# Optimization experiments

Hardware: AMD Instinct MI355X
Metric: run time of the kernel (lower is better)

The kernel has to match this reference:

```python
import jax, jax.numpy as jnp
import numpy as np

I, H = 1, 16  # input_size, hidden_size


def setup_inputs() -> dict:
    key = jax.random.key(0)
    ks = jax.random.split(key, 7)
    B, T = 8192, 512
    s_ih = 1.0 / np.sqrt(H)
    return {
        "x": jax.random.normal(ks[0], (B, T, I), dtype=jnp.float32),
        "W_ih": jax.random.uniform(ks[1], (3 * H, I), minval=-s_ih, maxval=s_ih, dtype=jnp.float32),
        "W_hh": jax.random.uniform(ks[2], (3 * H, H), minval=-s_ih, maxval=s_ih, dtype=jnp.float32),
        "b_ih": jax.random.uniform(ks[3], (3 * H,), minval=-s_ih, maxval=s_ih, dtype=jnp.float32),
        "b_hh": jax.random.uniform(ks[4], (3 * H,), minval=-s_ih, maxval=s_ih, dtype=jnp.float32),
        "fc_w": jax.random.uniform(ks[5], (1, H), minval=-s_ih, maxval=s_ih, dtype=jnp.float32),
        "fc_b": jax.random.uniform(ks[6], (1,), minval=-s_ih, maxval=s_ih, dtype=jnp.float32),
    }


def _gru_last_hidden(x, W_ih, W_hh, b_ih, b_hh):
    # Precompute input projections for all timesteps: [B, T, 3H]
    xp = jnp.einsum("bti,gi->btg", x, W_ih) + b_ih
    xp = jnp.transpose(xp, (1, 0, 2))  # [T, B, 3H] for scan over time
    B = x.shape[0]
    h0 = jnp.zeros((B, H), dtype=x.dtype)

    def step(h, xt):
        # PyTorch GRU gate equations (gate order: r, z, n)
        gh = h @ W_hh.T + b_hh  # [B, 3H]
        xr, xz, xn = xt[:, :H], xt[:, H:2 * H], xt[:, 2 * H:]
        hr, hz, hn = gh[:, :H], gh[:, H:2 * H], gh[:, 2 * H:]
        r = jax.nn.sigmoid(xr + hr)
        z = jax.nn.sigmoid(xz + hz)
        n = jnp.tanh(xn + r * hn)
        h_new = (1.0 - z) * n + z * h
        return h_new, None

    h_last, _ = jax.lax.scan(step, h0, xp)
    return h_last  # [B, H]


def reference(x, W_ih, W_hh, b_ih, b_hh, fc_w, fc_b):
    # Dropout is identity in eval mode
    h_last = _gru_last_hidden(x, W_ih, W_hh, b_ih, b_hh)
    return h_last @ fc_w.T + fc_b  # [B, 1]
```

## Files before the change

kernel.cpp:

```cpp
#include <hip/hip_runtime.h>

namespace {

constexpr int T_LEN = 512;
constexpr float LOG2E = 1.4426950408889634f;

typedef _Float16 half4 __attribute__((ext_vector_type(4)));
typedef _Float16 half2v __attribute__((ext_vector_type(2)));
typedef float v4f __attribute__((ext_vector_type(4)));

__device__ __forceinline__ float fexp2(float a) {
#if __has_builtin(__builtin_amdgcn_exp2f)
    return __builtin_amdgcn_exp2f(a);
#else
    return exp2f(a);
#endif
}

__device__ __forceinline__ v4f mfma16h(half4 a, half4 b, v4f c) {
#if __has_builtin(__builtin_amdgcn_mfma_f32_16x16x16f16)
    return __builtin_amdgcn_mfma_f32_16x16x16f16(a, b, c, 0, 0, 0);
#else
    v4f d;
    asm volatile("v_mfma_f32_16x16x16_f16 %0, %1, %2, %3\n\ts_nop 7\n\ts_nop 7"
                 : "=v"(d) : "v"(a), "v"(b), "v"(c));
    return d;
#endif
}

__device__ __forceinline__ unsigned pk_f16(float a, float b) {
#if __has_builtin(__builtin_amdgcn_cvt_pkrtz)
    return __builtin_bit_cast(unsigned, __builtin_amdgcn_cvt_pkrtz(a, b));
#else
    half2v r; r[0] = (_Float16)a; r[1] = (_Float16)b;
    return __builtin_bit_cast(unsigned, r);
#endif
}

template<int CTRL>
__device__ __forceinline__ unsigned dpp_mov_u(unsigned v) {
    return (unsigned)__builtin_amdgcn_mov_dpp((int)v, CTRL, 0xF, 0xF, false);
}

__device__ __forceinline__ float gru_pair(float drp, float dzp, float dnp,
                                          float xt, float wihn, float bihn,
                                          float hp) {
    float Er = fexp2(drp);
    float Ez = fexp2(dzp);
    float pr = 1.0f + Er;
    float pz = 1.0f + Ez;
    float ip = __builtin_amdgcn_rcpf(pr * pz);
    float r  = ip * pz;
    float z  = ip * pr;
    float xn = __builtin_fmaf(xt, wihn, bihn);
    float v  = __builtin_fmaf(r, dnp, xn);
    float n  = __builtin_fmaf(-2.0f, __builtin_amdgcn_rcpf(1.0f + fexp2(v)), 1.0f);
    return __builtin_fmaf(z, hp - n, n);
}

__global__ __launch_bounds__(64) void gru_mfma8d(
        const float* __restrict__ x,
        const float* __restrict__ W_ih,
        const float* __restrict__ W_hh,
        const float* __restrict__ b_ih,
        const float* __restrict__ b_hh,
        const float* __restrict__ fc_w,
        const float* __restrict__ fc_b,
        float* __restrict__ out) {
    const int L  = threadIdx.x;
    const int e  = L & 15;
    const int g  = L >> 4;
    const int jD = g * 4;
    const int ehi  = (e >> 3) & 1;
    const int ecol = e & 7;
    const int be   = blockIdx.x * 8 + ecol;
    const int r0   = jD + 2 * ehi;

    const float sR = -LOG2E;
    const float sN = 2.0f * LOG2E;

    half4 ar_h, az_h, an_h;
#pragma unroll
    for (int i = 0; i < 4; ++i) {
        ar_h[i] = (_Float16)(W_hh[(0  + e) * 16 + jD + i] * sR);
        az_h[i] = (_Float16)(W_hh[(16 + e) * 16 + jD + i] * sR);
        an_h[i] = (_Float16)(W_hh[(32 + e) * 16 + jD + i] * sN);
    }

    v4f c_r, c_z, c_n;
#pragma unroll
    for (int i = 0; i < 4; ++i) {
        int rj = jD + i;
        c_r[i] = (b_ih[rj]      + b_hh[rj])      * sR;
        c_z[i] = (b_ih[16 + rj] + b_hh[16 + rj]) * sR;
        c_n[i] = b_hh[32 + rj] * sN;
    }
    const float wihr0 = W_ih[r0]          * sR, wihr1 = W_ih[r0 + 1]      * sR;
    const float wihz0 = W_ih[16 + r0]     * sR, wihz1 = W_ih[16 + r0 + 1] * sR;
    const float wihn0 = W_ih[32 + r0]     * sN, wihn1 = W_ih[32 + r0 + 1] * sN;
    const float bihn0 = b_ih[32 + r0]     * sN, bihn1 = b_ih[32 + r0 + 1] * sN;

    const float4* xb = (const float4*)(x + (size_t)be * T_LEN);
    float4 xc0 = xb[0], xc1 = xb[1], xc2 = xb[2], xc3 = xb[3];

    float hp0 = 0.f, hp1 = 0.f;
    uint2 hz; hz.x = 0u; hz.y = 0u;
    half4 hf = __builtin_bit_cast(half4, hz);

#pragma unroll 1
    for (int c = 0; c < T_LEN / 16; ++c) {
        float4 xn0, xn1, xn2, xn3;
        if (c + 1 < T_LEN / 16) {
            xn0 = xb[(c + 1) * 4 + 0];
            xn1 = xb[(c + 1) * 4 + 1];
            xn2 = xb[(c + 1) * 4 + 2];
            xn3 = xb[(c + 1) * 4 + 3];
        }
#pragma unroll
        for (int s = 0; s < 16; ++s) {
            float4 q4 = (s < 4) ? xc0 : (s < 8) ? xc1 : (s < 12) ? xc2 : xc3;
            float xt  = ((s & 3) == 0) ? q4.x : ((s & 3) == 1) ? q4.y
                      : ((s & 3) == 2) ? q4.z : q4.w;

            v4f dr = mfma16h(ar_h, hf, c_r);
            v4f dz = mfma16h(az_h, hf, c_z);
            v4f dn = mfma16h(an_h, hf, c_n);

            float d_r0 = __builtin_fmaf(xt, wihr0, ehi ? dr[2] : dr[0]);
            float d_r1 = __builtin_fmaf(xt, wihr1, ehi ? dr[3] : dr[1]);
            float d_z0 = __builtin_fmaf(xt, wihz0, ehi ? dz[2] : dz[0]);
            float d_z1 = __builtin_fmaf(xt, wihz1, ehi ? dz[3] : dz[1]);
            float d_n0 = ehi ? dn[2] : dn[0];
            float d_n1 = ehi ? dn[3] : dn[1];

            float h0n = gru_pair(d_r0, d_z0, d_n0, xt, wihn0, bihn0, hp0);
            float h1n = gru_pair(d_r1, d_z1, d_n1, xt, wihn1, bihn1, hp1);
            hp0 = h0n; hp1 = h1n;

            unsigned mine = pk_f16(h0n, h1n);
            unsigned oth  = dpp_mov_u<0x128>(mine);
            uint2 hv;
            hv.x = ehi ? oth  : mine;
            hv.y = ehi ? mine : oth;
            hf = __builtin_bit_cast(half4, hv);
        }
        if (c + 1 < T_LEN / 16) { xc0 = xn0; xc1 = xn1; xc2 = xn2; xc3 = xn3; }
    }

    float p = hp0 * fc_w[r0] + hp1 * fc_w[r0 + 1];
    p += __shfl_xor(p, 8, 64);
    p += __shfl_xor(p, 16, 64);
    p += __shfl_xor(p, 32, 64);
    if (L < 8) out[blockIdx.x * 8 + L] = p + fc_b[0];
}

}

extern "C" void kernel_launch(void* const* d_in, const int* in_sizes, int n_in,
                              void* d_out, int out_size, void* d_ws, size_t ws_size,
                              hipStream_t stream) {
    const float* x    = (const float*)d_in[0];
    const float* W_ih = (const float*)d_in[1];
    const float* W_hh = (const float*)d_in[2];
    const float* b_ih = (const float*)d_in[3];
    const float* b_hh = (const float*)d_in[4];
    const float* fc_w = (const float*)d_in[5];
    const float* fc_b = (const float*)d_in[6];
    float* out = (float*)d_out;

    const int B = out_size;
    const int blocks = B / 8;
    gru_mfma8d<<<blocks, 64, 0, stream>>>(x, W_ih, W_hh, b_ih, b_hh,
                                          fc_w, fc_b, out);
}
```

Baseline: 87.68 us.

## Map one hidden unit per lane with 4 batch columns per wave

Each wave now processes 4 batch sequences instead of 8, so each lane computes a single hidden unit per step rather than two, and the grid doubles. The hidden-state transpose back into MFMA B-operand layout uses three DPP row shifts plus selects, with a runtime probe that detects the shift direction. This shortens the per-step serial gate chain and adds more waves to hide latency, at the cost of doubling total MFMA issue per batch element and adding more cross-lane moves.

```diff
diff --git a/kernel.cpp b/kernel.cpp
--- a/kernel.cpp
+++ b/kernel.cpp
@@ -38,8 +38,15 @@
 }
 
 template<int CTRL>
-__device__ __forceinline__ unsigned dpp_mov_u(unsigned v) {
-    return (unsigned)__builtin_amdgcn_mov_dpp((int)v, CTRL, 0xF, 0xF, false);
+__device__ __forceinline__ float dpp_mov_f(float v) {
+    return __builtin_bit_cast(float,
+        __builtin_amdgcn_mov_dpp(__builtin_bit_cast(int, v), CTRL, 0xF, 0xF, false));
+}
+
+__device__ __forceinline__ float sel4(v4f d, bool qb0, bool qb1) {
+    float a = qb0 ? d[1] : d[0];
+    float b = qb0 ? d[3] : d[2];
+    return qb1 ? b : a;
 }
 
 __device__ __forceinline__ float gru_pair(float drp, float dzp, float dnp,
@@ -58,7 +65,7 @@
     return __builtin_fmaf(z, hp - n, n);
 }
 
-__global__ __launch_bounds__(64) void gru_mfma8d(
+__global__ __launch_bounds__(64) void gru_mfma4d(
         const float* __restrict__ x,
         const float* __restrict__ W_ih,
         const float* __restrict__ W_hh,
@@ -71,10 +78,15 @@
     const int e  = L & 15;
     const int g  = L >> 4;
     const int jD = g * 4;
-    const int ehi  = (e >> 3) & 1;
-    const int ecol = e & 7;
-    const int be   = blockIdx.x * 8 + ecol;
-    const int r0   = jD + 2 * ehi;
+    const int q    = (e >> 2) & 3;
+    const bool qb0 = (q & 1) != 0;
+    const bool qb1 = (q & 2) != 0;
+    const int ecol = e & 3;
+    const int be   = blockIdx.x * 4 + ecol;
+    const int rme  = jD + q;
+
+    const int tprobe = __builtin_amdgcn_mov_dpp(e, 0x124, 0xF, 0xF, false);
+    const bool flip = (((tprobe - e) & 15) != 4);
 
     const float sR = -LOG2E;
     const float sN = 2.0f * LOG2E;
@@ -95,15 +107,15 @@
         c_z[i] = (b_ih[16 + rj] + b_hh[16 + rj]) * sR;
         c_n[i] = b_hh[32 + rj] * sN;
     }
-    const float wihr0 = W_ih[r0]          * sR, wihr1 = W_ih[r0 + 1]      * sR;
-    const float wihz0 = W_ih[16 + r0]     * sR, wihz1 = W_ih[16 + r0 + 1] * sR;
-    const float wihn0 = W_ih[32 + r0]     * sN, wihn1 = W_ih[32 + r0 + 1] * sN;
-    const float bihn0 = b_ih[32 + r0]     * sN, bihn1 = b_ih[32 + r0 + 1] * sN;
+    const float wihr_s = W_ih[rme]      * sR;
+    const float wihz_s = W_ih[16 + rme] * sR;
+    const float wihn_s = W_ih[32 + rme] * sN;
+    const float bihn_s = b_ih[32 + rme] * sN;
 
     const float4* xb = (const float4*)(x + (size_t)be * T_LEN);
     float4 xc0 = xb[0], xc1 = xb[1], xc2 = xb[2], xc3 = xb[3];
 
-    float hp0 = 0.f, hp1 = 0.f;
+    float hp = 0.f;
     uint2 hz; hz.x = 0u; hz.y = 0u;
     half4 hf = __builtin_bit_cast(half4, hz);
 
@@ -126,32 +138,40 @@
             v4f dz = mfma16h(az_h, hf, c_z);
             v4f dn = mfma16h(an_h, hf, c_n);
 
-            float d_r0 = __builtin_fmaf(xt, wihr0, ehi ? dr[2] : dr[0]);
-            float d_r1 = __builtin_fmaf(xt, wihr1, ehi ? dr[3] : dr[1]);
-            float d_z0 = __builtin_fmaf(xt, wihz0, ehi ? dz[2] : dz[0]);
-            float d_z1 = __builtin_fmaf(xt, wihz1, ehi ? dz[3] : dz[1]);
-            float d_n0 = ehi ? dn[2] : dn[0];
-            float d_n1 = ehi ? dn[3] : dn[1];
+            float d_r = __builtin_fmaf(xt, wihr_s, sel4(dr, qb0, qb1));
+            float d_z = __builtin_fmaf(xt, wihz_s, sel4(dz, qb0, qb1));
+            float d_n = sel4(dn, qb0, qb1);
+            float hn = gru_pair(d_r, d_z, d_n, xt, wihn_s, bihn_s, hp);
+            hp = hn;
 
-            float h0n = gru_pair(d_r0, d_z0, d_n0, xt, wihn0, bihn0, hp0);
-            float h1n = gru_pair(d_r1, d_z1, d_n1, xt, wihn1, bihn1, hp1);
-            hp0 = h0n; hp1 = h1n;
-
-            unsigned mine = pk_f16(h0n, h1n);
-            unsigned oth  = dpp_mov_u<0x128>(mine);
+            float v0 = hn;
+            float v1 = dpp_mov_f<0x124>(hn);
+            float v2 = dpp_mov_f<0x128>(hn);
+            float v3 = dpp_mov_f<0x12C>(hn);
+            float t1 = flip ? v3 : v1;
+            float t3 = flip ? v1 : v3;
+            float a0 = qb0 ? t3 : v0, b0 = qb0 ? t1 : v2;
+            float row0 = qb1 ? b0 : a0;
+            float a1 = qb0 ? v0 : t1, b1 = qb0 ? v2 : t3;
+            float row1 = qb1 ? b1 : a1;
+            float a2 = qb0 ? t1 : v2, b2 = qb0 ? t3 : v0;
+            float row2 = qb1 ? b2 : a2;
+            float a3 = qb0 ? v2 : t3, b3 = qb0 ? v0 : t1;
+            float row3 = qb1 ? b3 : a3;
             uint2 hv;
-            hv.x = ehi ? oth  : mine;
-            hv.y = ehi ? mine : oth;
+            hv.x = pk_f16(row0, row1);
+            hv.y = pk_f16(row2, row3);
             hf = __builtin_bit_cast(half4, hv);
         }
         if (c + 1 < T_LEN / 16) { xc0 = xn0; xc1 = xn1; xc2 = xn2; xc3 = xn3; }
     }
 
-    float p = hp0 * fc_w[r0] + hp1 * fc_w[r0 + 1];
+    float p = hp * fc_w[rme];
+    p += __shfl_xor(p, 4, 64);
     p += __shfl_xor(p, 8, 64);
     p += __shfl_xor(p, 16, 64);
     p += __shfl_xor(p, 32, 64);
-    if (L < 8) out[blockIdx.x * 8 + L] = p + fc_b[0];
+    if (L < 4) out[blockIdx.x * 4 + L] = p + fc_b[0];
 }
 
 }
@@ -169,7 +189,7 @@
     float* out = (float*)d_out;
 
     const int B = out_size;
-    const int blocks = B / 8;
-    gru_mfma8d<<<blocks, 64, 0, stream>>>(x, W_ih, W_hh, b_ih, b_hh,
+    const int blocks = B / 4;
+    gru_mfma4d<<<blocks, 64, 0, stream>>>(x, W_ih, W_hh, b_ih, b_hh,
                                           fc_w, fc_b, out);
 }
```

Measured after the change: 117.1 us. 1.34x slower.
